# Optimization experiments

Hardware: AMD Instinct MI355X
Metric: run time of the kernel (lower is better)

The kernel has to match this reference:

```python
import jax, jax.numpy as jnp
import numpy as np

HIDDEN_DIM = 4096
EXPANSION = 4
SINKHORN_ITERS = 20
EPS = 1e-05
ALPHA_INIT = 0.01


def setup_inputs() -> dict:
    key = jax.random.key(0)
    k_x, k_res = jax.random.split(key)
    x = jax.random.normal(k_x, (4096, EXPANSION, HIDDEN_DIM), dtype=jnp.float32)
    rmsnorm_weight = jnp.ones((HIDDEN_DIM,), dtype=jnp.bfloat16)
    H_pre = jnp.zeros((EXPANSION,), dtype=jnp.float32)
    H_post = jnp.zeros((EXPANSION,), dtype=jnp.float32)
    H_res = ALPHA_INIT * jax.random.normal(k_res, (EXPANSION, EXPANSION), dtype=jnp.float32)
    return {"x": x, "rmsnorm_weight": rmsnorm_weight, "H_pre": H_pre,
            "H_post": H_post, "H_res": H_res}


def reference(x, rmsnorm_weight, H_pre, H_post, H_res):
    x_f32 = x.astype(jnp.float32)  # [B, n, C]
    # Pre-mix aggregation over the n expanded streams
    H_pre_act = jax.nn.sigmoid(H_pre)
    x_agg = jnp.einsum('k,bkc->bc', H_pre_act, x_f32)  # [B, C]
    # bf16 round-trip as in the original (x_agg.bfloat16().float())
    x_agg_bf = x_agg.astype(jnp.bfloat16).astype(jnp.float32)
    rms = jnp.sqrt(jnp.mean(x_agg_bf * x_agg_bf, axis=-1, keepdims=True) + EPS)
    y_norm = x_agg_bf / rms * rmsnorm_weight.astype(jnp.float32)  # [B, C]
    # Sinkhorn normalization of the tiny n x n mixing matrix
    M0 = jnp.exp(H_res.astype(jnp.float32))
    def body(M, _):
        M = M / jnp.maximum(M.sum(axis=1, keepdims=True), EPS)
        M = M / jnp.maximum(M.sum(axis=0, keepdims=True), EPS)
        return M, None
    M, _ = jax.lax.scan(body, M0, None, length=SINKHORN_ITERS)
    H_post_act = 2.0 * jax.nn.sigmoid(H_post)
    # [B, n, C]: mixed residual streams + broadcast of normalized aggregate
    out = jnp.einsum('ij,bjc->bic', M, x_f32) + H_post_act[None, :, None] * y_norm[:, None, :]
    return out
```

## Files before the change

kernel.cpp:

```cpp
#include <hip/hip_runtime.h>
#include <hip/hip_bf16.h>

constexpr int C   = 4096;
constexpr int NE  = 4;
constexpr int B   = 4096;
constexpr int THREADS = 512;
constexpr int PER = C / THREADS;
constexpr float EPSV = 1e-5f;

__device__ inline float bf16_rne(float f) {
    unsigned int u = __float_as_uint(f);
    unsigned int r = (u + 0x7FFFu + ((u >> 16) & 1u)) & 0xFFFF0000u;
    return __uint_as_float(r);
}

__global__ __launch_bounds__(THREADS)
void mhc_fused(const float* __restrict__ x,
               const float* __restrict__ w,
               const float* __restrict__ Hpre,
               const float* __restrict__ Hpost,
               const float* __restrict__ Hres,
               float* __restrict__ out) {
    const int b   = blockIdx.x;
    const int tid = threadIdx.x;
    const size_t rowbase = (size_t)b * NE * C;
    const int c0 = tid * PER;

    float xs[NE][PER];
    #pragma unroll
    for (int k = 0; k < NE; ++k) {
        const float4* p = reinterpret_cast<const float4*>(x + rowbase + (size_t)k * C + c0);
        float4 a = p[0];
        float4 bq = p[1];
        xs[k][0] = a.x;  xs[k][1] = a.y;  xs[k][2] = a.z;  xs[k][3] = a.w;
        xs[k][4] = bq.x; xs[k][5] = bq.y; xs[k][6] = bq.z; xs[k][7] = bq.w;
    }

    __shared__ float sM[NE * NE];
    __shared__ float red[THREADS / 64];

    if (tid == 0) {
        float M[NE][NE];
        for (int i = 0; i < NE; ++i)
            for (int j = 0; j < NE; ++j)
                M[i][j] = expf(Hres[i * NE + j]);
        for (int it = 0; it < 20; ++it) {
            for (int i = 0; i < NE; ++i) {
                float rs = fmaxf(M[i][0] + M[i][1] + M[i][2] + M[i][3], EPSV);
                for (int j = 0; j < NE; ++j) M[i][j] /= rs;
            }
            for (int j = 0; j < NE; ++j) {
                float cs = fmaxf(M[0][j] + M[1][j] + M[2][j] + M[3][j], EPSV);
                for (int i = 0; i < NE; ++i) M[i][j] /= cs;
            }
        }
        for (int i = 0; i < NE; ++i)
            for (int j = 0; j < NE; ++j)
                sM[i * NE + j] = M[i][j];
    }

    const float s0 = 1.0f / (1.0f + expf(-Hpre[0]));
    const float s1 = 1.0f / (1.0f + expf(-Hpre[1]));
    const float s2 = 1.0f / (1.0f + expf(-Hpre[2]));
    const float s3 = 1.0f / (1.0f + expf(-Hpre[3]));
    float hp[NE];
    #pragma unroll
    for (int i = 0; i < NE; ++i) hp[i] = 2.0f / (1.0f + expf(-Hpost[i]));

    float aggbf[PER];
    float ss = 0.0f;
    #pragma unroll
    for (int c = 0; c < PER; ++c) {
        float a = s0 * xs[0][c] + s1 * xs[1][c] + s2 * xs[2][c] + s3 * xs[3][c];
        float abf = bf16_rne(a);
        aggbf[c] = abf;
        ss += abf * abf;
    }

    #pragma unroll
    for (int off = 32; off > 0; off >>= 1) ss += __shfl_xor(ss, off);
    const int lane = tid & 63;
    const int wid  = tid >> 6;
    if (lane == 0) red[wid] = ss;
    __syncthreads();
    float tot = 0.0f;
    #pragma unroll
    for (int i = 0; i < THREADS / 64; ++i) tot += red[i];

    const float rinv = 1.0f / sqrtf(tot * (1.0f / (float)C) + EPSV);

    float y[PER];
    {
        const float4* pw = reinterpret_cast<const float4*>(w + c0);
        float4 w0 = pw[0];
        float4 w1 = pw[1];
        y[0] = aggbf[0] * rinv * w0.x;  y[1] = aggbf[1] * rinv * w0.y;
        y[2] = aggbf[2] * rinv * w0.z;  y[3] = aggbf[3] * rinv * w0.w;
        y[4] = aggbf[4] * rinv * w1.x;  y[5] = aggbf[5] * rinv * w1.y;
        y[6] = aggbf[6] * rinv * w1.z;  y[7] = aggbf[7] * rinv * w1.w;
    }

    float M[NE][NE];
    #pragma unroll
    for (int i = 0; i < NE; ++i)
        #pragma unroll
        for (int j = 0; j < NE; ++j)
            M[i][j] = sM[i * NE + j];

    #pragma unroll
    for (int i = 0; i < NE; ++i) {
        float o[PER];
        #pragma unroll
        for (int c = 0; c < PER; ++c) {
            o[c] = M[i][0] * xs[0][c] + M[i][1] * xs[1][c]
                 + M[i][2] * xs[2][c] + M[i][3] * xs[3][c]
                 + hp[i] * y[c];
        }
        float4* po = reinterpret_cast<float4*>(out + rowbase + (size_t)i * C + c0);
        po[0] = make_float4(o[0], o[1], o[2], o[3]);
        po[1] = make_float4(o[4], o[5], o[6], o[7]);
    }
}

extern "C" void kernel_launch(void* const* d_in, const int* in_sizes, int n_in,
                              void* d_out, int out_size, void* d_ws, size_t ws_size,
                              hipStream_t stream) {
    const float* x     = (const float*)d_in[0];
    const float* w     = (const float*)d_in[1];
    const float* Hpre  = (const float*)d_in[2];
    const float* Hpost = (const float*)d_in[3];
    const float* Hres  = (const float*)d_in[4];
    float* out         = (float*)d_out;

    mhc_fused<<<B, THREADS, 0, stream>>>(x, w, Hpre, Hpost, Hres, out);
}
```

Measured before the change: 130.3 us.

## Hoist Sinkhorn and gate activations into a separate prep kernel

Moves the per-block serial Sinkhorn iteration (run by thread 0 in every one of 4096 blocks) and the sigmoid gate computations into a single tiny prep kernel that uses wave shuffles and writes results to workspace. The main kernel then just loads 24 floats from workspace. This removes redundant serial work and the latency it adds to each block before the reduction barrier, at the cost of an extra kernel launch.

```diff
diff --git a/kernel.cpp b/kernel.cpp
--- a/kernel.cpp
+++ b/kernel.cpp
@@ -14,13 +14,32 @@
     return __uint_as_float(r);
 }
 
+__global__ void mhc_prep(const float* __restrict__ Hpre,
+                         const float* __restrict__ Hpost,
+                         const float* __restrict__ Hres,
+                         float* __restrict__ ws) {
+    const int l = threadIdx.x;
+    float m = (l < 16) ? expf(Hres[l]) : 0.0f;
+    for (int it = 0; it < 20; ++it) {
+        float r = m + __shfl_xor(m, 1);
+        r += __shfl_xor(r, 2);
+        m /= fmaxf(r, EPSV);
+        float cs = m + __shfl_xor(m, 4);
+        cs += __shfl_xor(cs, 8);
+        m /= fmaxf(cs, EPSV);
+    }
+    if (l < 16) ws[l] = m;
+    if (l < NE) {
+        ws[16 + l] = 1.0f / (1.0f + expf(-Hpre[l]));
+        ws[20 + l] = 2.0f / (1.0f + expf(-Hpost[l]));
+    }
+}
+
 __global__ __launch_bounds__(THREADS)
-void mhc_fused(const float* __restrict__ x,
-               const float* __restrict__ w,
-               const float* __restrict__ Hpre,
-               const float* __restrict__ Hpost,
-               const float* __restrict__ Hres,
-               float* __restrict__ out) {
+void mhc_main(const float* __restrict__ x,
+              const float* __restrict__ w,
+              const float* __restrict__ ws,
+              float* __restrict__ out) {
     const int b   = blockIdx.x;
     const int tid = threadIdx.x;
     const size_t rowbase = (size_t)b * NE * C;
@@ -36,36 +55,16 @@
         xs[k][4] = bq.x; xs[k][5] = bq.y; xs[k][6] = bq.z; xs[k][7] = bq.w;
     }
 
-    __shared__ float sM[NE * NE];
-    __shared__ float red[THREADS / 64];
-
-    if (tid == 0) {
-        float M[NE][NE];
-        for (int i = 0; i < NE; ++i)
-            for (int j = 0; j < NE; ++j)
-                M[i][j] = expf(Hres[i * NE + j]);
-        for (int it = 0; it < 20; ++it) {
-            for (int i = 0; i < NE; ++i) {
-                float rs = fmaxf(M[i][0] + M[i][1] + M[i][2] + M[i][3], EPSV);
-                for (int j = 0; j < NE; ++j) M[i][j] /= rs;
-            }
-            for (int j = 0; j < NE; ++j) {
-                float cs = fmaxf(M[0][j] + M[1][j] + M[2][j] + M[3][j], EPSV);
-                for (int i = 0; i < NE; ++i) M[i][j] /= cs;
-            }
-        }
-        for (int i = 0; i < NE; ++i)
-            for (int j = 0; j < NE; ++j)
-                sM[i * NE + j] = M[i][j];
-    }
-
-    const float s0 = 1.0f / (1.0f + expf(-Hpre[0]));
-    const float s1 = 1.0f / (1.0f + expf(-Hpre[1]));
-    const float s2 = 1.0f / (1.0f + expf(-Hpre[2]));
-    const float s3 = 1.0f / (1.0f + expf(-Hpre[3]));
+    const float s0 = ws[16], s1 = ws[17], s2 = ws[18], s3 = ws[19];
     float hp[NE];
     #pragma unroll
-    for (int i = 0; i < NE; ++i) hp[i] = 2.0f / (1.0f + expf(-Hpost[i]));
+    for (int i = 0; i < NE; ++i) hp[i] = ws[20 + i];
+    float M[NE][NE];
+    #pragma unroll
+    for (int i = 0; i < NE; ++i)
+        #pragma unroll
+        for (int j = 0; j < NE; ++j)
+            M[i][j] = ws[i * NE + j];
 
     float aggbf[PER];
     float ss = 0.0f;
@@ -79,6 +78,7 @@
 
     #pragma unroll
     for (int off = 32; off > 0; off >>= 1) ss += __shfl_xor(ss, off);
+    __shared__ float red[THREADS / 64];
     const int lane = tid & 63;
     const int wid  = tid >> 6;
     if (lane == 0) red[wid] = ss;
@@ -99,13 +99,6 @@
         y[4] = aggbf[4] * rinv * w1.x;  y[5] = aggbf[5] * rinv * w1.y;
         y[6] = aggbf[6] * rinv * w1.z;  y[7] = aggbf[7] * rinv * w1.w;
     }
-
-    float M[NE][NE];
-    #pragma unroll
-    for (int i = 0; i < NE; ++i)
-        #pragma unroll
-        for (int j = 0; j < NE; ++j)
-            M[i][j] = sM[i * NE + j];
 
     #pragma unroll
     for (int i = 0; i < NE; ++i) {
@@ -131,6 +124,8 @@
     const float* Hpost = (const float*)d_in[3];
     const float* Hres  = (const float*)d_in[4];
     float* out         = (float*)d_out;
+    float* ws          = (float*)d_ws;
 
-    mhc_fused<<<B, THREADS, 0, stream>>>(x, w, Hpre, Hpost, Hres, out);
+    mhc_prep<<<1, 64, 0, stream>>>(Hpre, Hpost, Hres, ws);
+    mhc_main<<<B, THREADS, 0, stream>>>(x, w, ws, out);
 }
```

Measured after the change: 113.1 us. -13.2%, faster.
